# Optimization experiments

Hardware: AMD Instinct MI355X
Metric: run time of the kernel (lower is better)

Reference implementation:

```python
import jax, jax.numpy as jnp
import numpy as np

N = 262144          # total views (rows of x)
G = 65536           # number of objects / view-groups (len(n_views))
D_IN, D_MID, D_GAT, D_OUT = 512, 256, 128, 256
BN_EPS = 1e-5
L2_EPS = 1e-9


def setup_inputs() -> dict:
    key = jax.random.key(0)
    ks = jax.random.split(key, 12)
    # post-backbone pooled features (dla34 last stage -> AdaptiveMaxPool2d(1) -> flatten)
    x = jax.random.normal(ks[0], (N, D_IN), jnp.float32)
    # ragged grouping: sorted segment ids, every segment guaranteed non-empty
    extra = jax.random.randint(ks[1], (N - G,), 0, G)
    seg_ids = jnp.sort(jnp.concatenate([jnp.arange(G), extra]).astype(jnp.int32))
    # sv_enc2: Linear(512,256) + BatchNorm1d (eval stats) + ReLU
    w2 = jax.random.normal(ks[2], (D_IN, D_MID), jnp.float32) * (D_IN ** -0.5)
    b2 = jnp.zeros((D_MID,), jnp.float32)
    bn_g = jnp.ones((D_MID,), jnp.float32)
    bn_b = jnp.zeros((D_MID,), jnp.float32)
    bn_m = jnp.zeros((D_MID,), jnp.float32)
    bn_v = jnp.ones((D_MID,), jnp.float32)
    # sv_enc3: Linear(256,128) + ReLU
    w3 = jax.random.normal(ks[3], (D_MID, D_GAT), jnp.float32) * (D_MID ** -0.5)
    b3 = jnp.zeros((D_GAT,), jnp.float32)
    # SelfGraphAttentionLinear(128, residual=True, dynamic_batching=True):
    # per-group attention pooling with residual
    gw = jax.random.normal(ks[4], (D_GAT, D_GAT), jnp.float32) * (D_GAT ** -0.5)
    gb = jnp.zeros((D_GAT,), jnp.float32)
    ga = jax.random.normal(ks[5], (D_GAT,), jnp.float32) * (D_GAT ** -0.5)
    # projection_head: Linear(128, 256), no activation
    pw = jax.random.normal(ks[6], (D_GAT, D_OUT), jnp.float32) * (D_GAT ** -0.5)
    pb = jnp.zeros((D_OUT,), jnp.float32)
    return {"x": x, "seg_ids": seg_ids, "w2": w2, "b2": b2,
            "bn_g": bn_g, "bn_b": bn_b, "bn_m": bn_m, "bn_v": bn_v,
            "w3": w3, "b3": b3, "gw": gw, "gb": gb, "ga": ga,
            "pw": pw, "pb": pb}


def reference(x, seg_ids, w2, b2, bn_g, bn_b, bn_m, bn_v, w3, b3, gw, gb, ga, pw, pb):
    # sv_enc2: Linear -> BN(eval) -> ReLU
    h = x @ w2 + b2
    h = bn_g * (h - bn_m) * jax.lax.rsqrt(bn_v + BN_EPS) + bn_b
    h = jax.nn.relu(h)
    # sv_enc3: Linear -> ReLU  -> [N, 128]
    h = jax.nn.relu(h @ w3 + b3)
    # GAT with dynamic batching: per-segment softmax attention pooling + residual
    g = h @ gw + gb                                    # [N, 128]
    e = g @ ga                                         # [N] attention logits
    m = jax.ops.segment_max(e, seg_ids, num_segments=G)
    w = jnp.exp(e - m[seg_ids])
    den = jax.ops.segment_sum(w, seg_ids, num_segments=G)
    alpha = w / den[seg_ids]                           # segment softmax
    pooled = jax.ops.segment_sum(alpha[:, None] * g, seg_ids, num_segments=G)
    h = jax.nn.relu(h + pooled[seg_ids])               # residual + gat_act
    # ragged per-group max pooling (the python loop in the original)
    obj = jax.ops.segment_max(h, seg_ids, num_segments=G)  # [G, 128]
    # projection head + L2 normalization
    out = obj @ pw + pb
    out = out / (jnp.linalg.norm(out, axis=1, keepdims=True) + L2_EPS)
    return out
```

## Files before the change

kernel.cpp:

```cpp
#include <hip/hip_runtime.h>
#include <hip/hip_bf16.h>
#include <stdint.h>

typedef __bf16 bf16;
typedef __bf16 bf16x2 __attribute__((ext_vector_type(2)));
typedef __bf16 bf16x4 __attribute__((ext_vector_type(4)));
typedef __bf16 bf16x8 __attribute__((ext_vector_type(8)));
typedef float  f32x4  __attribute__((ext_vector_type(4)));
typedef float  f32x2  __attribute__((ext_vector_type(2)));

#define NROWS 262144
#define GSEG  65536
#define DIN   512
#define DMID  256
#define DGAT  128
#define DOUT  256

#define OFF_W2S   0u
#define OFF_W3T   262144u
#define OFF_GWT   327680u
#define OFF_PWT   360448u
#define OFF_BNS   425984u
#define OFF_BNB   427008u
#define OFF_RS    428032u
#define OFF_H2    1048576u
#define OFF_G     68157440u
#define OFF_E     135266304u

#define GLOAD16(gptr, lptr) __builtin_amdgcn_global_load_lds( \
    (const __attribute__((address_space(1))) void*)(gptr),    \
    (__attribute__((address_space(3))) void*)(lptr), 16, 0, 0)

__global__ __launch_bounds__(256) void k_prep(
    const float* __restrict__ w2, const float* __restrict__ w3, const float* __restrict__ gw,
    const float* __restrict__ pw,
    const float* __restrict__ b2, const float* __restrict__ bn_g, const float* __restrict__ bn_b,
    const float* __restrict__ bn_m, const float* __restrict__ bn_v,
    bf16* __restrict__ w2s, bf16* __restrict__ w3t, bf16* __restrict__ gwt,
    bf16* __restrict__ pwt, float* __restrict__ bnS, float* __restrict__ bnB) {
  int idx = blockIdx.x * 256 + threadIdx.x;
  if (idx < DIN * DMID) {
    int k = idx / DMID, c = idx % DMID;
    int kk = k & 63, kb = k & ~63;
    w2s[c * DIN + kb + (kk ^ ((c & 7) << 3))] = (bf16)w2[idx];
  }
  if (idx < DMID * DGAT) {
    int k = idx / DGAT, c = idx % DGAT;
    w3t[c * DMID + k] = (bf16)w3[idx];
  }
  if (idx < DGAT * DGAT) {
    int k = idx / DGAT, c = idx % DGAT;
    gwt[c * DGAT + k] = (bf16)gw[idx];
  }
  if (idx < DOUT * DGAT) {
    int c = idx >> 7, k = idx & 127;
    pwt[idx] = (bf16)pw[k * DOUT + c];
  }
  if (idx < DMID) {
    float s = bn_g[idx] * rsqrtf(bn_v[idx] + 1e-5f);
    bnS[idx] = s;
    bnB[idx] = s * (b2[idx] - bn_m[idx]) + bn_b[idx];
  }
}

__global__ __launch_bounds__(256) void k_rowstart(const int* __restrict__ seg, int* __restrict__ rs) {
  int i = blockIdx.x * 256 + threadIdx.x;
  if (i >= NROWS) return;
  int s = seg[i];
  if (i == 0) rs[s] = 0;
  else if (seg[i - 1] != s) rs[s] = i;
  if (i == NROWS - 1) rs[GSEG] = NROWS;
}

__global__ __launch_bounds__(256, 2) void k_enc(
    const float* __restrict__ x, const bf16* __restrict__ w2s,
    const bf16* __restrict__ w3t, const bf16* __restrict__ gwt,
    const float* __restrict__ bnS, const float* __restrict__ bnB,
    const float* __restrict__ b3, const float* __restrict__ gb, const float* __restrict__ ga,
    bf16* __restrict__ h2, bf16* __restrict__ g, float* __restrict__ e) {
  __shared__ bf16 u[32768];
  __shared__ float eP[256];
  bf16* As  = u;
  bf16* Bs  = u + 8192;
  bf16* H1s = u;
  bf16* Hs  = u;
  bf16* Gs  = u + 16384;
  const int t = threadIdx.x;
  const int mBase = blockIdx.x * 128;
  const int w = t >> 6, l = t & 63;
  const int wm = w >> 1, wn = w & 1;
  const int l15 = l & 15, lh = l >> 4;
  const f32x4 zero = {0.f, 0.f, 0.f, 0.f};

  const int ar = t >> 1;
  const int ak = (t & 1) * 32;
  const float* xp = x + (size_t)(mBase + ar) * DIN + ak;
  const int aswz = (ar & 7) << 3;
  const int bcol0 = w * 64 + (l >> 3);
  const int bkk = (l & 7) * 8;

  f32x4 acc[4][8];
#pragma unroll
  for (int m = 0; m < 4; m++)
#pragma unroll
    for (int n = 0; n < 8; n++) acc[m][n] = zero;

  float4 pf[8];
#pragma unroll
  for (int j = 0; j < 8; j++) pf[j] = *(const float4*)(xp + j * 4);

  for (int kt = 0; kt < 8; ++kt) {
    bf16x8 av[4];
#pragma unroll
    for (int j = 0; j < 4; j++) {
      av[j][0] = (bf16)pf[2 * j].x; av[j][1] = (bf16)pf[2 * j].y;
      av[j][2] = (bf16)pf[2 * j].z; av[j][3] = (bf16)pf[2 * j].w;
      av[j][4] = (bf16)pf[2 * j + 1].x; av[j][5] = (bf16)pf[2 * j + 1].y;
      av[j][6] = (bf16)pf[2 * j + 1].z; av[j][7] = (bf16)pf[2 * j + 1].w;
    }
    __syncthreads();
#pragma unroll
    for (int j = 0; j < 4; j++)
      *(bf16x8*)(As + ar * 64 + ((ak + 8 * j) ^ aswz)) = av[j];
#pragma unroll
    for (int i = 0; i < 8; i++) {
      GLOAD16(w2s + (size_t)(bcol0 + i * 8) * DIN + kt * 64 + bkk,
              Bs + (w * 8 + i) * 512);
    }
    __syncthreads();
    if (kt < 7) {
#pragma unroll
      for (int j = 0; j < 8; j++) pf[j] = *(const float4*)(xp + (kt + 1) * 64 + j * 4);
    }
#pragma unroll
    for (int ks = 0; ks < 2; ++ks) {
      const int kofs = ks * 32 + lh * 8;
      bf16x8 a[4], b[8];
#pragma unroll
      for (int m = 0; m < 4; m++) {
        int r = wm * 64 + m * 16 + l15;
        a[m] = *(const bf16x8*)(As + r * 64 + (kofs ^ ((r & 7) << 3)));
      }
#pragma unroll
      for (int n = 0; n < 8; n++) {
        int c = wn * 128 + n * 16 + l15;
        b[n] = *(const bf16x8*)(Bs + c * 64 + (kofs ^ ((c & 7) << 3)));
      }
#pragma unroll
      for (int m = 0; m < 4; m++)
#pragma unroll
        for (int n = 0; n < 8; n++)
          acc[m][n] = __builtin_amdgcn_mfma_f32_16x16x32_bf16(b[n], a[m], acc[m][n], 0, 0, 0);
    }
  }
  __syncthreads();

  const int rsw = (l15 & 7) << 3;
#pragma unroll
  for (int n = 0; n < 8; n++) {
    int c0 = wn * 128 + n * 16 + lh * 4;
    f32x4 s4 = *(const f32x4*)(bnS + c0);
    f32x4 b4 = *(const f32x4*)(bnB + c0);
    int cs = (c0 & ~63) + ((c0 & 63) ^ rsw);
#pragma unroll
    for (int m = 0; m < 4; m++) {
      int rl = wm * 64 + m * 16 + l15;
      bf16x4 o;
#pragma unroll
      for (int q = 0; q < 4; q++) {
        float v = acc[m][n][q] * s4[q] + b4[q];
        o[q] = (bf16)(v > 0.f ? v : 0.f);
      }
      *(bf16x4*)(H1s + rl * 256 + cs) = o;
    }
  }
  __syncthreads();

  f32x4 acc2[4][4];
#pragma unroll
  for (int m = 0; m < 4; m++)
#pragma unroll
    for (int n = 0; n < 4; n++) acc2[m][n] = zero;
#pragma unroll
  for (int ks = 0; ks < 8; ++ks) {
    const int kofs = ks * 32 + lh * 8;
    const int kb = kofs & ~63, kk = kofs & 63;
    bf16x8 a[4], b[4];
#pragma unroll
    for (int n = 0; n < 4; n++) {
      int c = wn * 64 + n * 16 + l15;
      b[n] = *(const bf16x8*)(w3t + (size_t)c * DMID + kofs);
    }
#pragma unroll
    for (int m = 0; m < 4; m++) {
      int r = wm * 64 + m * 16 + l15;
      a[m] = *(const bf16x8*)(H1s + r * 256 + kb + (kk ^ ((r & 7) << 3)));
    }
#pragma unroll
    for (int m = 0; m < 4; m++)
#pragma unroll
      for (int n = 0; n < 4; n++)
        acc2[m][n] = __builtin_amdgcn_mfma_f32_16x16x32_bf16(b[n], a[m], acc2[m][n], 0, 0, 0);
  }
  __syncthreads();

#pragma unroll
  for (int n = 0; n < 4; n++) {
    int c0 = wn * 64 + n * 16 + lh * 4;
    f32x4 b4 = *(const f32x4*)(b3 + c0);
#pragma unroll
    for (int m = 0; m < 4; m++) {
      int rl = wm * 64 + m * 16 + l15;
      bf16x4 hb;
#pragma unroll
      for (int q = 0; q < 4; q++) {
        float v = acc2[m][n][q] + b4[q];
        hb[q] = (bf16)(v > 0.f ? v : 0.f);
      }
      *(bf16x4*)(Hs + rl * 128 + (c0 ^ ((rl & 7) << 3))) = hb;
    }
  }
  __syncthreads();

  f32x4 gacc[4][4];
#pragma unroll
  for (int m = 0; m < 4; m++)
#pragma unroll
    for (int n = 0; n < 4; n++) gacc[m][n] = zero;
#pragma unroll
  for (int ks = 0; ks < 4; ++ks) {
    const int kofs = ks * 32 + lh * 8;
    bf16x8 a[4], b[4];
#pragma unroll
    for (int n = 0; n < 4; n++) {
      int c = wn * 64 + n * 16 + l15;
      b[n] = *(const bf16x8*)(gwt + (size_t)c * DGAT + kofs);
    }
#pragma unroll
    for (int m = 0; m < 4; m++) {
      int r = wm * 64 + m * 16 + l15;
      a[m] = *(const bf16x8*)(Hs + r * 128 + (kofs ^ ((r & 7) << 3)));
    }
#pragma unroll
    for (int m = 0; m < 4; m++)
#pragma unroll
      for (int n = 0; n < 4; n++)
        gacc[m][n] = __builtin_amdgcn_mfma_f32_16x16x32_bf16(b[n], a[m], gacc[m][n], 0, 0, 0);
  }
  float ep[4] = {0.f, 0.f, 0.f, 0.f};
#pragma unroll
  for (int n = 0; n < 4; n++) {
    int c0 = wn * 64 + n * 16 + lh * 4;
    f32x4 gb4 = *(const f32x4*)(gb + c0);
    f32x4 ga4 = *(const f32x4*)(ga + c0);
#pragma unroll
    for (int m = 0; m < 4; m++) {
      int rl = wm * 64 + m * 16 + l15;
      bf16x4 gv;
#pragma unroll
      for (int q = 0; q < 4; q++) gv[q] = (bf16)(gacc[m][n][q] + gb4[q]);
      *(bf16x4*)(Gs + rl * 128 + (c0 ^ ((rl & 7) << 3))) = gv;
#pragma unroll
      for (int q = 0; q < 4; q++) ep[m] += (float)gv[q] * ga4[q];
    }
  }
#pragma unroll
  for (int m = 0; m < 4; m++) {
    float v = ep[m];
    v += __shfl_xor(v, 16, 64);
    v += __shfl_xor(v, 32, 64);
    if (l < 16) eP[(wm * 64 + m * 16 + l) * 2 + wn] = v;
  }
  __syncthreads();

  const int drow = t >> 4;
  const int dc = (t & 15) * 8;
#pragma unroll
  for (int i = 0; i < 8; ++i) {
    int rl = i * 16 + drow;
    int cs = dc ^ ((rl & 7) << 3);
    *(bf16x8*)(h2 + (size_t)(mBase + rl) * DGAT + dc) = *(const bf16x8*)(Hs + rl * 128 + cs);
    *(bf16x8*)(g  + (size_t)(mBase + rl) * DGAT + dc) = *(const bf16x8*)(Gs + rl * 128 + cs);
  }
  if (t < 128) e[mBase + t] = eP[t * 2] + eP[t * 2 + 1];
}

__global__ __launch_bounds__(256) void k_segproj(
    const float* __restrict__ e, const bf16* __restrict__ g, const bf16* __restrict__ h2,
    const int* __restrict__ rs, const bf16* __restrict__ pwt, const float* __restrict__ pb,
    float* __restrict__ out) {
  __shared__ bf16 objs[16 * 128];
  __shared__ float red[16 * 4];
  const int t = threadIdx.x;
  const int w = t >> 6, l = t & 63;
  const int l15 = l & 15, lh = l >> 4;
  const int gBase = blockIdx.x * 16;
  const f32x4 zero = {0.f, 0.f, 0.f, 0.f};

#pragma unroll
  for (int j = 0; j < 4; ++j) {
    const int sl = w * 4 + j;
    const int s = gBase + sl;
    const int r0 = rs[s], r1 = rs[s + 1];
    float m = -3.4e38f;
    for (int r = r0; r < r1; ++r) m = fmaxf(m, e[r]);
    float den = 0.f;
    f32x2 p = {0.f, 0.f};
    for (int r = r0; r < r1; ++r) {
      float wr = __expf(e[r] - m);
      den += wr;
      bf16x2 gv = *(const bf16x2*)(g + (size_t)r * DGAT + l * 2);
      p[0] += wr * (float)gv[0];
      p[1] += wr * (float)gv[1];
    }
    float inv = 1.f / den;
    p[0] *= inv; p[1] *= inv;
    f32x2 om = {0.f, 0.f};
    for (int r = r0; r < r1; ++r) {
      bf16x2 hv = *(const bf16x2*)(h2 + (size_t)r * DGAT + l * 2);
      om[0] = fmaxf(om[0], fmaxf((float)hv[0] + p[0], 0.f));
      om[1] = fmaxf(om[1], fmaxf((float)hv[1] + p[1], 0.f));
    }
    bf16x2 ob;
    ob[0] = (bf16)om[0];
    ob[1] = (bf16)om[1];
    int k2 = (l * 2) ^ ((sl & 7) << 3);
    *(bf16x2*)(objs + sl * 128 + k2) = ob;
  }
  __syncthreads();

  f32x4 acc[4];
#pragma unroll
  for (int n = 0; n < 4; n++) acc[n] = zero;
#pragma unroll
  for (int ks = 0; ks < 4; ++ks) {
    const int kofs = ks * 32 + lh * 8;
    bf16x8 a = *(const bf16x8*)(objs + l15 * 128 + (kofs ^ ((l15 & 7) << 3)));
#pragma unroll
    for (int n = 0; n < 4; n++) {
      int c = w * 64 + n * 16 + l15;
      bf16x8 b = *(const bf16x8*)(pwt + (size_t)c * DGAT + kofs);
      acc[n] = __builtin_amdgcn_mfma_f32_16x16x32_bf16(b, a, acc[n], 0, 0, 0);
    }
  }
  float s2 = 0.f;
#pragma unroll
  for (int n = 0; n < 4; n++) {
    int c0 = w * 64 + n * 16 + lh * 4;
    f32x4 p4 = *(const f32x4*)(pb + c0);
#pragma unroll
    for (int q = 0; q < 4; q++) {
      acc[n][q] += p4[q];
      s2 += acc[n][q] * acc[n][q];
    }
  }
  s2 += __shfl_xor(s2, 16, 64);
  s2 += __shfl_xor(s2, 32, 64);
  if (l < 16) red[l * 4 + w] = s2;
  __syncthreads();
  float tot = red[l15 * 4 + 0] + red[l15 * 4 + 1] + red[l15 * 4 + 2] + red[l15 * 4 + 3];
  float rinv = 1.f / (sqrtf(tot) + 1e-9f);
#pragma unroll
  for (int n = 0; n < 4; n++) {
    int c0 = w * 64 + n * 16 + lh * 4;
    f32x4 o;
#pragma unroll
    for (int q = 0; q < 4; q++) o[q] = acc[n][q] * rinv;
    *(f32x4*)(out + (size_t)(gBase + l15) * DOUT + c0) = o;
  }
}

extern "C" void kernel_launch(void* const* d_in, const int* in_sizes, int n_in,
                              void* d_out, int out_size, void* d_ws, size_t ws_size,
                              hipStream_t stream) {
  const float* x    = (const float*)d_in[0];
  const int*   seg  = (const int*)d_in[1];
  const float* w2   = (const float*)d_in[2];
  const float* b2   = (const float*)d_in[3];
  const float* bn_g = (const float*)d_in[4];
  const float* bn_b = (const float*)d_in[5];
  const float* bn_m = (const float*)d_in[6];
  const float* bn_v = (const float*)d_in[7];
  const float* w3   = (const float*)d_in[8];
  const float* b3   = (const float*)d_in[9];
  const float* gw   = (const float*)d_in[10];
  const float* gb   = (const float*)d_in[11];
  const float* ga   = (const float*)d_in[12];
  const float* pw   = (const float*)d_in[13];
  const float* pb   = (const float*)d_in[14];

  char* ws = (char*)d_ws;
  bf16*  w2s = (bf16*)(ws + OFF_W2S);
  bf16*  w3t = (bf16*)(ws + OFF_W3T);
  bf16*  gwt = (bf16*)(ws + OFF_GWT);
  bf16*  pwt = (bf16*)(ws + OFF_PWT);
  float* bnS = (float*)(ws + OFF_BNS);
  float* bnB = (float*)(ws + OFF_BNB);
  int*   rs  = (int*)(ws + OFF_RS);
  bf16*  h2  = (bf16*)(ws + OFF_H2);
  bf16*  g   = (bf16*)(ws + OFF_G);
  float* e   = (float*)(ws + OFF_E);
  float* out = (float*)d_out;

  k_prep<<<512, 256, 0, stream>>>(w2, w3, gw, pw, b2, bn_g, bn_b, bn_m, bn_v,
                                  w2s, w3t, gwt, pwt, bnS, bnB);
  k_rowstart<<<NROWS / 256, 256, 0, stream>>>(seg, rs);
  k_enc<<<NROWS / 128, 256, 0, stream>>>(x, w2s, w3t, gwt, bnS, bnB, b3, gb, ga, h2, g, e);
  k_segproj<<<GSEG / 16, 256, 0, stream>>>(e, g, h2, rs, pwt, pb, out);
}
```

Measured before the change: 339.3 us.

## Halve encoder row tile to raise occupancy; use online softmax in segment pooling

The fused encoder kernel now processes 64 rows per block instead of 128, with a smaller accumulator set, reduced shared memory and a launch bound of 3 blocks per CU. This is meant to improve latency hiding. In exchange, the W2 tile is reloaded twice as often per row and each block does less MMA work. The segment pooling loop also replaces its separate max pass with an online-softmax rescaling, saving one read of the logits per segment at the cost of an extra exp per row.

```diff
diff --git a/kernel.cpp b/kernel.cpp
--- a/kernel.cpp
+++ b/kernel.cpp
@@ -72,56 +72,55 @@
   if (i == NROWS - 1) rs[GSEG] = NROWS;
 }
 
-__global__ __launch_bounds__(256, 2) void k_enc(
+__global__ __launch_bounds__(256, 3) void k_enc(
     const float* __restrict__ x, const bf16* __restrict__ w2s,
     const bf16* __restrict__ w3t, const bf16* __restrict__ gwt,
     const float* __restrict__ bnS, const float* __restrict__ bnB,
     const float* __restrict__ b3, const float* __restrict__ gb, const float* __restrict__ ga,
     bf16* __restrict__ h2, bf16* __restrict__ g, float* __restrict__ e) {
-  __shared__ bf16 u[32768];
-  __shared__ float eP[256];
+  __shared__ bf16 u[24576];
+  __shared__ float eP[128];
   bf16* As  = u;
-  bf16* Bs  = u + 8192;
+  bf16* Bs  = u + 4096;
   bf16* H1s = u;
-  bf16* Hs  = u;
-  bf16* Gs  = u + 16384;
+  bf16* Hs  = u + 16384;
+  bf16* Gs  = u;
   const int t = threadIdx.x;
-  const int mBase = blockIdx.x * 128;
+  const int mBase = blockIdx.x * 64;
   const int w = t >> 6, l = t & 63;
   const int wm = w >> 1, wn = w & 1;
   const int l15 = l & 15, lh = l >> 4;
   const f32x4 zero = {0.f, 0.f, 0.f, 0.f};
 
-  const int ar = t >> 1;
-  const int ak = (t & 1) * 32;
+  const int ar = t >> 2;
+  const int ak = (t & 3) * 16;
   const float* xp = x + (size_t)(mBase + ar) * DIN + ak;
   const int aswz = (ar & 7) << 3;
   const int bcol0 = w * 64 + (l >> 3);
   const int bkk = (l & 7) * 8;
 
-  f32x4 acc[4][8];
+  f32x4 acc[4][4];
 #pragma unroll
   for (int m = 0; m < 4; m++)
 #pragma unroll
-    for (int n = 0; n < 8; n++) acc[m][n] = zero;
-
-  float4 pf[8];
-#pragma unroll
-  for (int j = 0; j < 8; j++) pf[j] = *(const float4*)(xp + j * 4);
+    for (int n = 0; n < 4; n++) acc[m][n] = zero;
+
+  float4 pf[4];
+#pragma unroll
+  for (int j = 0; j < 4; j++) pf[j] = *(const float4*)(xp + j * 4);
 
   for (int kt = 0; kt < 8; ++kt) {
-    bf16x8 av[4];
-#pragma unroll
-    for (int j = 0; j < 4; j++) {
+    bf16x8 av[2];
+#pragma unroll
+    for (int j = 0; j < 2; j++) {
       av[j][0] = (bf16)pf[2 * j].x; av[j][1] = (bf16)pf[2 * j].y;
       av[j][2] = (bf16)pf[2 * j].z; av[j][3] = (bf16)pf[2 * j].w;
       av[j][4] = (bf16)pf[2 * j + 1].x; av[j][5] = (bf16)pf[2 * j + 1].y;
       av[j][6] = (bf16)pf[2 * j + 1].z; av[j][7] = (bf16)pf[2 * j + 1].w;
     }
     __syncthreads();
-#pragma unroll
-    for (int j = 0; j < 4; j++)
-      *(bf16x8*)(As + ar * 64 + ((ak + 8 * j) ^ aswz)) = av[j];
+    *(bf16x8*)(As + ar * 64 + ((ak + 0) ^ aswz)) = av[0];
+    *(bf16x8*)(As + ar * 64 + ((ak + 8) ^ aswz)) = av[1];
 #pragma unroll
     for (int i = 0; i < 8; i++) {
       GLOAD16(w2s + (size_t)(bcol0 + i * 8) * DIN + kt * 64 + bkk,
@@ -130,26 +129,26 @@
     __syncthreads();
     if (kt < 7) {
 #pragma unroll
-      for (int j = 0; j < 8; j++) pf[j] = *(const float4*)(xp + (kt + 1) * 64 + j * 4);
+      for (int j = 0; j < 4; j++) pf[j] = *(const float4*)(xp + (kt + 1) * 64 + j * 4);
     }
 #pragma unroll
     for (int ks = 0; ks < 2; ++ks) {
       const int kofs = ks * 32 + lh * 8;
-      bf16x8 a[4], b[8];
+      bf16x8 a[4], b[4];
 #pragma unroll
       for (int m = 0; m < 4; m++) {
-        int r = wm * 64 + m * 16 + l15;
+        int r = m * 16 + l15;
         a[m] = *(const bf16x8*)(As + r * 64 + (kofs ^ ((r & 7) << 3)));
       }
 #pragma unroll
-      for (int n = 0; n < 8; n++) {
-        int c = wn * 128 + n * 16 + l15;
+      for (int n = 0; n < 4; n++) {
+        int c = w * 64 + n * 16 + l15;
         b[n] = *(const bf16x8*)(Bs + c * 64 + (kofs ^ ((c & 7) << 3)));
       }
 #pragma unroll
       for (int m = 0; m < 4; m++)
 #pragma unroll
-        for (int n = 0; n < 8; n++)
+        for (int n = 0; n < 4; n++)
           acc[m][n] = __builtin_amdgcn_mfma_f32_16x16x32_bf16(b[n], a[m], acc[m][n], 0, 0, 0);
     }
   }
@@ -157,14 +156,14 @@
 
   const int rsw = (l15 & 7) << 3;
 #pragma unroll
-  for (int n = 0; n < 8; n++) {
-    int c0 = wn * 128 + n * 16 + lh * 4;
+  for (int n = 0; n < 4; n++) {
+    int c0 = w * 64 + n * 16 + lh * 4;
     f32x4 s4 = *(const f32x4*)(bnS + c0);
     f32x4 b4 = *(const f32x4*)(bnB + c0);
     int cs = (c0 & ~63) + ((c0 & 63) ^ rsw);
 #pragma unroll
     for (int m = 0; m < 4; m++) {
-      int rl = wm * 64 + m * 16 + l15;
+      int rl = m * 16 + l15;
       bf16x4 o;
 #pragma unroll
       for (int q = 0; q < 4; q++) {
@@ -176,41 +175,39 @@
   }
   __syncthreads();
 
-  f32x4 acc2[4][4];
-#pragma unroll
-  for (int m = 0; m < 4; m++)
+  f32x4 acc2[2][4];
+#pragma unroll
+  for (int m = 0; m < 2; m++)
 #pragma unroll
     for (int n = 0; n < 4; n++) acc2[m][n] = zero;
 #pragma unroll
   for (int ks = 0; ks < 8; ++ks) {
     const int kofs = ks * 32 + lh * 8;
     const int kb = kofs & ~63, kk = kofs & 63;
-    bf16x8 a[4], b[4];
+    bf16x8 a[2], b[4];
 #pragma unroll
     for (int n = 0; n < 4; n++) {
       int c = wn * 64 + n * 16 + l15;
       b[n] = *(const bf16x8*)(w3t + (size_t)c * DMID + kofs);
     }
 #pragma unroll
-    for (int m = 0; m < 4; m++) {
-      int r = wm * 64 + m * 16 + l15;
+    for (int m = 0; m < 2; m++) {
+      int r = wm * 32 + m * 16 + l15;
       a[m] = *(const bf16x8*)(H1s + r * 256 + kb + (kk ^ ((r & 7) << 3)));
     }
 #pragma unroll
-    for (int m = 0; m < 4; m++)
+    for (int m = 0; m < 2; m++)
 #pragma unroll
       for (int n = 0; n < 4; n++)
         acc2[m][n] = __builtin_amdgcn_mfma_f32_16x16x32_bf16(b[n], a[m], acc2[m][n], 0, 0, 0);
   }
-  __syncthreads();
-
 #pragma unroll
   for (int n = 0; n < 4; n++) {
     int c0 = wn * 64 + n * 16 + lh * 4;
     f32x4 b4 = *(const f32x4*)(b3 + c0);
 #pragma unroll
-    for (int m = 0; m < 4; m++) {
-      int rl = wm * 64 + m * 16 + l15;
+    for (int m = 0; m < 2; m++) {
+      int rl = wm * 32 + m * 16 + l15;
       bf16x4 hb;
 #pragma unroll
       for (int q = 0; q < 4; q++) {
@@ -222,40 +219,40 @@
   }
   __syncthreads();
 
-  f32x4 gacc[4][4];
-#pragma unroll
-  for (int m = 0; m < 4; m++)
+  f32x4 gacc[2][4];
+#pragma unroll
+  for (int m = 0; m < 2; m++)
 #pragma unroll
     for (int n = 0; n < 4; n++) gacc[m][n] = zero;
 #pragma unroll
   for (int ks = 0; ks < 4; ++ks) {
     const int kofs = ks * 32 + lh * 8;
-    bf16x8 a[4], b[4];
+    bf16x8 a[2], b[4];
 #pragma unroll
     for (int n = 0; n < 4; n++) {
       int c = wn * 64 + n * 16 + l15;
       b[n] = *(const bf16x8*)(gwt + (size_t)c * DGAT + kofs);
     }
 #pragma unroll
-    for (int m = 0; m < 4; m++) {
-      int r = wm * 64 + m * 16 + l15;
+    for (int m = 0; m < 2; m++) {
+      int r = wm * 32 + m * 16 + l15;
       a[m] = *(const bf16x8*)(Hs + r * 128 + (kofs ^ ((r & 7) << 3)));
     }
 #pragma unroll
-    for (int m = 0; m < 4; m++)
+    for (int m = 0; m < 2; m++)
 #pragma unroll
       for (int n = 0; n < 4; n++)
         gacc[m][n] = __builtin_amdgcn_mfma_f32_16x16x32_bf16(b[n], a[m], gacc[m][n], 0, 0, 0);
   }
-  float ep[4] = {0.f, 0.f, 0.f, 0.f};
+  float ep[2] = {0.f, 0.f};
 #pragma unroll
   for (int n = 0; n < 4; n++) {
     int c0 = wn * 64 + n * 16 + lh * 4;
     f32x4 gb4 = *(const f32x4*)(gb + c0);
     f32x4 ga4 = *(const f32x4*)(ga + c0);
 #pragma unroll
-    for (int m = 0; m < 4; m++) {
-      int rl = wm * 64 + m * 16 + l15;
+    for (int m = 0; m < 2; m++) {
+      int rl = wm * 32 + m * 16 + l15;
       bf16x4 gv;
 #pragma unroll
       for (int q = 0; q < 4; q++) gv[q] = (bf16)(gacc[m][n][q] + gb4[q]);
@@ -265,24 +262,24 @@
     }
   }
 #pragma unroll
-  for (int m = 0; m < 4; m++) {
+  for (int m = 0; m < 2; m++) {
     float v = ep[m];
     v += __shfl_xor(v, 16, 64);
     v += __shfl_xor(v, 32, 64);
-    if (l < 16) eP[(wm * 64 + m * 16 + l) * 2 + wn] = v;
+    if (l < 16) eP[(wm * 32 + m * 16 + l) * 2 + wn] = v;
   }
   __syncthreads();
 
   const int drow = t >> 4;
   const int dc = (t & 15) * 8;
 #pragma unroll
-  for (int i = 0; i < 8; ++i) {
+  for (int i = 0; i < 4; ++i) {
     int rl = i * 16 + drow;
     int cs = dc ^ ((rl & 7) << 3);
     *(bf16x8*)(h2 + (size_t)(mBase + rl) * DGAT + dc) = *(const bf16x8*)(Hs + rl * 128 + cs);
     *(bf16x8*)(g  + (size_t)(mBase + rl) * DGAT + dc) = *(const bf16x8*)(Gs + rl * 128 + cs);
   }
-  if (t < 128) e[mBase + t] = eP[t * 2] + eP[t * 2 + 1];
+  if (t < 64) e[mBase + t] = eP[t * 2] + eP[t * 2 + 1];
 }
 
 __global__ __launch_bounds__(256) void k_segproj(
@@ -302,16 +299,18 @@
     const int sl = w * 4 + j;
     const int s = gBase + sl;
     const int r0 = rs[s], r1 = rs[s + 1];
-    float m = -3.4e38f;
-    for (int r = r0; r < r1; ++r) m = fmaxf(m, e[r]);
-    float den = 0.f;
+    float m = -3.4e38f, den = 0.f;
     f32x2 p = {0.f, 0.f};
     for (int r = r0; r < r1; ++r) {
-      float wr = __expf(e[r] - m);
-      den += wr;
+      float ev = e[r];
+      float mn = fmaxf(m, ev);
+      float cor = __expf(m - mn);
+      float wr = __expf(ev - mn);
+      den = den * cor + wr;
       bf16x2 gv = *(const bf16x2*)(g + (size_t)r * DGAT + l * 2);
-      p[0] += wr * (float)gv[0];
-      p[1] += wr * (float)gv[1];
+      p[0] = p[0] * cor + wr * (float)gv[0];
+      p[1] = p[1] * cor + wr * (float)gv[1];
+      m = mn;
     }
     float inv = 1.f / den;
     p[0] *= inv; p[1] *= inv;
@@ -405,6 +404,6 @@
   k_prep<<<512, 256, 0, stream>>>(w2, w3, gw, pw, b2, bn_g, bn_b, bn_m, bn_v,
                                   w2s, w3t, gwt, pwt, bnS, bnB);
   k_rowstart<<<NROWS / 256, 256, 0, stream>>>(seg, rs);
-  k_enc<<<NROWS / 128, 256, 0, stream>>>(x, w2s, w3t, gwt, bnS, bnB, b3, gb, ga, h2, g, e);
+  k_enc<<<NROWS / 64, 256, 0, stream>>>(x, w2s, w3t, gwt, bnS, bnB, b3, gb, ga, h2, g, e);
   k_segproj<<<GSEG / 16, 256, 0, stream>>>(e, g, h2, rs, pwt, pb, out);
 }
```

Measured after the change: 343.7 us. About the same (+1.3%).
